# Optimization experiments

Measured on AMD Instinct MI355X. Metric: run time of the kernel, lower is better.

The kernel has to match this reference:

```python
import jax, jax.numpy as jnp
import numpy as np

BATCH, SEQ, HIDDEN = 8, 4096, 1024

def setup_inputs() -> dict:
    key = jax.random.key(0)
    hidden_states = jax.random.normal(key, (BATCH, SEQ, HIDDEN), dtype=jnp.float32)
    return {"hidden_states": hidden_states}

def reference(hidden_states) -> jnp.ndarray:
    # FFT along the sequence axis with orthonormal normalization (1/sqrt(N)),
    # then keep only the real part (FNet-style Fourier token mixing).
    fft_out = jnp.fft.fft(hidden_states, axis=1, norm="ortho")
    return jnp.real(fft_out).astype(hidden_states.dtype)
```

## Files before the change

### kernel.cpp

```cpp
#include <hip/hip_runtime.h>
#include <hip/hip_fp16.h>


static constexpr int SEQ = 4096;
static constexpr int HID = 1024;

struct alignas(8) h2x2 { __half2 a, b; };

__device__ __forceinline__ int rev4_3(int r) {
    return ((r & 3) << 4) | (r & 12) | ((r >> 4) & 3);
}


__device__ __forceinline__ void fft8(float* xr, float* xi) {
    const float C = 0.70710678118654752f;
    float ar[8], ai[8];
    ar[0] = xr[0] + xr[4];  ai[0] = xi[0] + xi[4];
    ar[1] = xr[0] - xr[4];  ai[1] = xi[0] - xi[4];
    ar[2] = xr[2] + xr[6];  ai[2] = xi[2] + xi[6];
    ar[3] = xr[2] - xr[6];  ai[3] = xi[2] - xi[6];
    ar[4] = xr[1] + xr[5];  ai[4] = xi[1] + xi[5];
    ar[5] = xr[1] - xr[5];  ai[5] = xi[1] - xi[5];
    ar[6] = xr[3] + xr[7];  ai[6] = xi[3] + xi[7];
    ar[7] = xr[3] - xr[7];  ai[7] = xi[3] - xi[7];
    float br[8], bi[8];
    br[0] = ar[0] + ar[2];  bi[0] = ai[0] + ai[2];
    br[2] = ar[0] - ar[2];  bi[2] = ai[0] - ai[2];
    br[1] = ar[1] + ai[3];  bi[1] = ai[1] - ar[3];
    br[3] = ar[1] - ai[3];  bi[3] = ai[1] + ar[3];
    br[4] = ar[4] + ar[6];  bi[4] = ai[4] + ai[6];
    br[6] = ar[4] - ar[6];  bi[6] = ai[4] - ai[6];
    br[5] = ar[5] + ai[7];  bi[5] = ai[5] - ar[7];
    br[7] = ar[5] - ai[7];  bi[7] = ai[5] + ar[7];
    const float t0r = br[4],                 t0i = bi[4];
    const float t1r = C * (br[5] + bi[5]),   t1i = C * (bi[5] - br[5]);
    const float t2r = bi[6],                 t2i = -br[6];
    const float t3r = C * (bi[7] - br[7]),   t3i = -C * (br[7] + bi[7]);
    xr[0] = br[0] + t0r;  xi[0] = bi[0] + t0i;
    xr[4] = br[0] - t0r;  xi[4] = bi[0] - t0i;
    xr[1] = br[1] + t1r;  xi[1] = bi[1] + t1i;
    xr[5] = br[1] - t1r;  xi[5] = bi[1] - t1i;
    xr[2] = br[2] + t2r;  xi[2] = bi[2] + t2i;
    xr[6] = br[2] - t2r;  xi[6] = bi[2] - t2i;
    xr[3] = br[3] + t3r;  xi[3] = bi[3] + t3i;
    xr[7] = br[3] - t3r;  xi[7] = bi[3] - t3i;
}

__device__ __forceinline__ void twiddle_chain(float* xr, float* xi,
                                              const float wc, const float ws) {
    float cr = wc, ci = ws;
    #pragma unroll
    for (int k = 1; k < 8; ++k) {
        const float tr = xr[k] * cr - xi[k] * ci;
        xi[k] = xr[k] * ci + xi[k] * cr;
        xr[k] = tr;
        if (k < 7) {
            const float nr = cr * wc - ci * ws;
            const float ni = cr * ws + ci * wc;
            cr = nr;  ci = ni;
        }
    }
}


__global__ __launch_bounds__(256) void fft_pass1_r8(const float* __restrict__ x,
                                                    __half2* __restrict__ u) {
    __shared__ float2 zs[2112];
    const int t  = threadIdx.x;
    const int pc = blockIdx.x & 15;
    const int n2 = (blockIdx.x >> 4) & 63;
    const int b  = blockIdx.x >> 10;
    const int c  = t & 31;
    const int q  = t >> 5;

    const float* xb = x + (size_t)b * SEQ * HID + (size_t)(pc * 64 + 2 * c);
    float xr[8], xi[8];
    #pragma unroll
    for (int a = 0; a < 8; ++a) {
        const float2 v = *(const float2*)(xb + (size_t)(n2 + 64 * (8 * a + q)) * HID);
        xr[a] = v.x;  xi[a] = v.y;
    }
    fft8(xr, xi);
    {
        float wsn, wcs;
        __sincosf(-0.09817477042468103f * (float)q, &wsn, &wcs);
        twiddle_chain(xr, xi, wcs, wsn);
    }
    #pragma unroll
    for (int k = 0; k < 8; ++k)
        zs[(k * 8 + q) * 33 + c] = make_float2(xr[k], xi[k]);
    __syncthreads();
    #pragma unroll
    for (int r = 0; r < 8; ++r) {
        const float2 v = zs[(q * 8 + r) * 33 + c];
        xr[r] = v.x;  xi[r] = v.y;
    }
    fft8(xr, xi);

    const float tw = -1.5339807878856412e-3f;
    float w0c, w0s, wsc, wss;
    __sincosf(tw * (float)(n2 * q), &w0s, &w0c);
    __sincosf(tw * (float)(n2 * 8), &wss, &wsc);
    const float sc = 0.015625f;
    w0c *= sc;  w0s *= sc;
    __half2* ub = u + (size_t)b * SEQ * 512 + (size_t)(64 * n2 + q) * 512 + pc * 32 + c;
    #pragma unroll
    for (int kh = 0; kh < 8; ++kh) {
        const float orr = xr[kh] * w0c - xi[kh] * w0s;
        const float oii = xr[kh] * w0s + xi[kh] * w0c;
        ub[(size_t)(8 * kh) * 512] = __floats2half2_rn(orr, oii);
        if (kh < 7) {
            const float nc = w0c * wsc - w0s * wss;
            const float ns = w0c * wss + w0s * wsc;
            w0c = nc;  w0s = ns;
        }
    }
}

__global__ __launch_bounds__(256) void fft_pass2_r8(const __half2* __restrict__ u,
                                                    float* __restrict__ out) {
    __shared__ float2 vs[2176];
    const int t   = threadIdx.x;
    const int b   = blockIdx.x >> 10;
    const int idx = blockIdx.x & 1023;
    const __half2* ub = u   + (size_t)b * SEQ * 512;
    float*         ob = out + (size_t)b * SEQ * HID;
    const float scale = 0.5f;
    float xr[8], xi[8];

    if (idx < 992) {
        const int k1 = 1 + (idx >> 5);
        const int pc = idx & 31;
        const int ab = t >> 7;
        const int q  = (t >> 4) & 7;
        const int c  = t & 15;
        const int k1sel = ab ? 64 - k1 : k1;
        const int p  = pc * 16 + c;
        const __half2* up = ub + (size_t)k1sel * 512 + p;
        #pragma unroll
        for (int a = 0; a < 8; ++a) {
            const float2 v = __half22float2(up[(size_t)(64 * (8 * a + q)) * 512]);
            xr[a] = v.x;  xi[a] = v.y;
        }
        fft8(xr, xi);
        {
            float wsn, wcs;
            __sincosf(-0.09817477042468103f * (float)q, &wsn, &wcs);
            twiddle_chain(xr, xi, wcs, wsn);
        }
        const int base = ab * 64;
        #pragma unroll
        for (int k = 0; k < 8; ++k)
            vs[(base + k * 8 + q) * 17 + c] = make_float2(xr[k], xi[k]);
        __syncthreads();
        #pragma unroll
        for (int r = 0; r < 8; ++r) {
            const float2 v = vs[(base + q * 8 + r) * 17 + c];
            xr[r] = v.x;  xi[r] = v.y;
        }
        fft8(xr, xi);
        __syncthreads();
        #pragma unroll
        for (int k = 0; k < 8; ++k)
            vs[(base + k * 8 + q) * 17 + c] = make_float2(xr[k], xi[k]);
        __syncthreads();
        float* op = ob + (size_t)k1sel * HID + 2 * p;
        #pragma unroll
        for (int kh = 0; kh < 8; ++kh) {
            const float2 pv = vs[((64 - base) + (7 - kh) * 8 + (7 - q)) * 17 + c];
            const int k2 = q + 8 * kh;
            *(float2*)(op + (size_t)(64 * k2) * HID) =
                make_float2((xr[kh] + pv.x) * scale, (xi[kh] + pv.y) * scale);
        }
    } else {
        const int s  = idx - 992;
        const int k1 = (s >> 4) * 32;
        const int pc = s & 15;
        const int q  = t >> 5;
        const int c  = t & 31;
        const int p  = pc * 32 + c;
        const __half2* up = ub + (size_t)k1 * 512 + p;
        #pragma unroll
        for (int a = 0; a < 8; ++a) {
            const float2 v = __half22float2(up[(size_t)(64 * (8 * a + q)) * 512]);
            xr[a] = v.x;  xi[a] = v.y;
        }
        fft8(xr, xi);
        {
            float wsn, wcs;
            __sincosf(-0.09817477042468103f * (float)q, &wsn, &wcs);
            twiddle_chain(xr, xi, wcs, wsn);
        }
        #pragma unroll
        for (int k = 0; k < 8; ++k)
            vs[(k * 8 + q) * 33 + c] = make_float2(xr[k], xi[k]);
        __syncthreads();
        #pragma unroll
        for (int r = 0; r < 8; ++r) {
            const float2 v = vs[(q * 8 + r) * 33 + c];
            xr[r] = v.x;  xi[r] = v.y;
        }
        fft8(xr, xi);
        __syncthreads();
        #pragma unroll
        for (int k = 0; k < 8; ++k)
            vs[(k * 8 + q) * 33 + c] = make_float2(xr[k], xi[k]);
        __syncthreads();
        const int q2 = (k1 == 0) ? ((8 - q) & 7) : (7 - q);
        float* op = ob + (size_t)k1 * HID + 2 * p;
        #pragma unroll
        for (int kh = 0; kh < 8; ++kh) {
            const int kh2 = (k1 == 0 && q == 0) ? ((8 - kh) & 7) : (7 - kh);
            const float2 pv = vs[(kh2 * 8 + q2) * 33 + c];
            const int k2 = q + 8 * kh;
            *(float2*)(op + (size_t)(64 * k2) * HID) =
                make_float2((xr[kh] + pv.x) * scale, (xi[kh] + pv.y) * scale);
        }
    }
}


template <int MC>
__device__ __forceinline__ void fft64_lds(float* re, float* im, int off, int stride, int mbase) {
    #pragma unroll
    for (int s = 0; s < 3; ++s) {
        const int L = 1 << (2 * s);
        const float ang = -6.283185307179586f / (float)(4 * L);
        #pragma unroll
        for (int mi = 0; mi < MC; ++mi) {
            const int m  = mbase + mi;
            const int j  = m & (L - 1);
            const int i0 = ((m >> (2 * s)) << (2 * s + 2)) + j;
            const int a0 = (i0        ) * stride + off;
            const int a1 = (i0 +     L) * stride + off;
            const int a2 = (i0 + 2 * L) * stride + off;
            const int a3 = (i0 + 3 * L) * stride + off;
            const float e0x = re[a0], e0y = im[a0];
            const float e1x = re[a1], e1y = im[a1];
            const float e2x = re[a2], e2y = im[a2];
            const float e3x = re[a3], e3y = im[a3];
            float w1s, w1c;
            __sincosf(ang * (float)j, &w1s, &w1c);
            const float w2c = w1c * w1c - w1s * w1s, w2s = 2.f * w1c * w1s;
            const float w3c = w2c * w1c - w2s * w1s, w3s = w2c * w1s + w2s * w1c;
            const float t1x = e1x * w1c - e1y * w1s, t1y = e1x * w1s + e1y * w1c;
            const float t2x = e2x * w2c - e2y * w2s, t2y = e2x * w2s + e2y * w2c;
            const float t3x = e3x * w3c - e3y * w3s, t3y = e3x * w3s + e3y * w3c;
            const float a02x = e0x + t2x, a02y = e0y + t2y;
            const float s02x = e0x - t2x, s02y = e0y - t2y;
            const float a13x = t1x + t3x, a13y = t1y + t3y;
            const float s13x = t1x - t3x, s13y = t1y - t3y;
            re[a0] = a02x + a13x;  im[a0] = a02y + a13y;
            re[a1] = s02x + s13y;  im[a1] = s02y - s13x;
            re[a2] = a02x - a13x;  im[a2] = a02y - a13y;
            re[a3] = s02x - s13y;  im[a3] = s02y + s13x;
        }
        __syncthreads();
    }
}

__global__ __launch_bounds__(256) void fft_pass1(const float* __restrict__ x,
                                                 float* __restrict__ out) {
    __shared__ float sre[64 * 65];
    __shared__ float sim[64 * 65];
    const int t  = threadIdx.x;
    const int pc = blockIdx.x & 7;
    const int n2 = (blockIdx.x >> 3) & 63;
    const int b  = blockIdx.x >> 9;
    const float* xb = x   + (size_t)b * SEQ * HID + pc * 128;
    float*       ob = out + (size_t)b * SEQ * HID + pc * 128;

    const int c  = t & 31;
    const int r0 = t >> 5;
    #pragma unroll
    for (int i = 0; i < 8; ++i) {
        const int r  = r0 + 8 * i;
        const float4 f = *(const float4*)(xb + (size_t)(n2 + 64 * r) * HID + 4 * c);
        const int rr = rev4_3(r);
        sre[rr * 65 + 2 * c]     = f.x;  sim[rr * 65 + 2 * c]     = f.y;
        sre[rr * 65 + 2 * c + 1] = f.z;  sim[rr * 65 + 2 * c + 1] = f.w;
    }
    __syncthreads();

    fft64_lds<4>(sre, sim, t & 63, 65, 4 * (t >> 6));

    const float tw = -1.5339807878856412e-3f;
    #pragma unroll
    for (int i = 0; i < 8; ++i) {
        const int k1 = r0 + 8 * i;
        float ws, wc;
        __sincosf(tw * (float)(n2 * k1), &ws, &wc);
        const float ar = sre[k1 * 65 + 2 * c],     ai = sim[k1 * 65 + 2 * c];
        const float br = sre[k1 * 65 + 2 * c + 1], bi = sim[k1 * 65 + 2 * c + 1];
        float4 f;
        f.x = ar * wc - ai * ws;  f.y = ar * ws + ai * wc;
        f.z = br * wc - bi * ws;  f.w = br * ws + bi * wc;
        *(float4*)(ob + (size_t)(64 * n2 + k1) * HID + 4 * c) = f;
    }
}

__global__ __launch_bounds__(256) void fft_pass2(float* out) {
    __shared__ float lds[8448];
    const int t   = threadIdx.x;
    const int b   = blockIdx.x >> 9;
    const int idx = blockIdx.x & 511;
    float* ob = out + (size_t)b * SEQ * HID;
    const float scale = 1.0f / 128.0f;

    if (idx < 496) {
        const int k1 = 1 + (idx >> 4);
        const int pc = idx & 15;
        float* are = lds;          float* aim = lds + 2112;
        float* bre = lds + 4224;   float* bim = lds + 6336;
        const int c  = t & 15;
        const int rg = t >> 4;
        #pragma unroll
        for (int i = 0; i < 4; ++i) {
            const int n2 = rg + 16 * i;
            const int rr = rev4_3(n2);
            const float4 fa = *(const float4*)(ob + (size_t)(64 * n2 + k1)      * HID + pc * 64 + 4 * c);
            const float4 fb = *(const float4*)(ob + (size_t)(64 * n2 + 64 - k1) * HID + pc * 64 + 4 * c);
            are[rr * 33 + 2 * c]     = fa.x;  aim[rr * 33 + 2 * c]     = fa.y;
            are[rr * 33 + 2 * c + 1] = fa.z;  aim[rr * 33 + 2 * c + 1] = fa.w;
            bre[rr * 33 + 2 * c]     = fb.x;  bim[rr * 33 + 2 * c]     = fb.y;
            bre[rr * 33 + 2 * c + 1] = fb.z;  bim[rr * 33 + 2 * c + 1] = fb.w;
        }
        __syncthreads();

        const int lane = t & 63;
        float* fre = lds + 4224 * (lane >> 5);
        fft64_lds<4>(fre, fre + 2112, lane & 31, 33, 4 * (t >> 6));

        #pragma unroll
        for (int i = 0; i < 4; ++i) {
            const int k2 = rg + 16 * i;
            const int q  = 63 - k2;
            float4 f, g;
            f.x = (are[k2 * 33 + 2 * c]     + bre[q * 33 + 2 * c])     * scale;
            f.y = (aim[k2 * 33 + 2 * c]     + bim[q * 33 + 2 * c])     * scale;
            f.z = (are[k2 * 33 + 2 * c + 1] + bre[q * 33 + 2 * c + 1]) * scale;
            f.w = (aim[k2 * 33 + 2 * c + 1] + bim[q * 33 + 2 * c + 1]) * scale;
            *(float4*)(ob + (size_t)(k1 + 64 * k2)      * HID + pc * 64 + 4 * c) = f;
            g.x = (bre[k2 * 33 + 2 * c]     + are[q * 33 + 2 * c])     * scale;
            g.y = (bim[k2 * 33 + 2 * c]     + aim[q * 33 + 2 * c])     * scale;
            g.z = (bre[k2 * 33 + 2 * c + 1] + are[q * 33 + 2 * c + 1]) * scale;
            g.w = (bim[k2 * 33 + 2 * c + 1] + aim[q * 33 + 2 * c + 1]) * scale;
            *(float4*)(ob + (size_t)(64 - k1 + 64 * k2) * HID + pc * 64 + 4 * c) = g;
        }
    } else {
        const int s  = idx - 496;
        const int k1 = (s >> 3) * 32;
        const int pc = s & 7;
        float* sre = lds;
        float* sim = lds + 4160;
        const int c  = t & 31;
        const int rg = t >> 5;
        #pragma unroll
        for (int i = 0; i < 8; ++i) {
            const int n2 = rg + 8 * i;
            const int rr = rev4_3(n2);
            const float4 f = *(const float4*)(ob + (size_t)(64 * n2 + k1) * HID + pc * 128 + 4 * c);
            sre[rr * 65 + 2 * c]     = f.x;  sim[rr * 65 + 2 * c]     = f.y;
            sre[rr * 65 + 2 * c + 1] = f.z;  sim[rr * 65 + 2 * c + 1] = f.w;
        }
        __syncthreads();

        fft64_lds<4>(sre, sim, t & 63, 65, 4 * (t >> 6));

        #pragma unroll
        for (int i = 0; i < 8; ++i) {
            const int k2 = rg + 8 * i;
            const int q  = (k1 == 0) ? ((64 - k2) & 63) : (63 - k2);
            float4 f;
            f.x = (sre[k2 * 65 + 2 * c]     + sre[q * 65 + 2 * c])     * scale;
            f.y = (sim[k2 * 65 + 2 * c]     + sim[q * 65 + 2 * c])     * scale;
            f.z = (sre[k2 * 65 + 2 * c + 1] + sre[q * 65 + 2 * c + 1]) * scale;
            f.w = (sim[k2 * 65 + 2 * c + 1] + sim[q * 65 + 2 * c + 1]) * scale;
            *(float4*)(ob + (size_t)(k1 + 64 * k2) * HID + pc * 128 + 4 * c) = f;
        }
    }
}

extern "C" void kernel_launch(void* const* d_in, const int* in_sizes, int n_in,
                              void* d_out, int out_size, void* d_ws, size_t ws_size,
                              hipStream_t stream) {
    const float* x = (const float*)d_in[0];
    float* out = (float*)d_out;
    const size_t need = (size_t)8 * SEQ * 512 * sizeof(__half2);
    if (ws_size >= need) {
        __half2* u = (__half2*)d_ws;
        fft_pass1_r8<<<dim3(8 * 64 * 16), dim3(256), 0, stream>>>(x, u);
        fft_pass2_r8<<<dim3(8 * 1024), dim3(256), 0, stream>>>(u, out);
    } else {
        fft_pass1<<<dim3(8 * 64 * 8), dim3(256), 0, stream>>>(x, out);
        fft_pass2<<<dim3(8 * 512), dim3(256), 0, stream>>>(out);
    }
}
```

Baseline: 263.9 us.

## Process two columns per thread with wider vector loads and nontemporal stores

Both FFT passes now have each thread handle two complex columns (two packed pairs). This allows 16-byte float4 global loads and stores, and 8-byte half2x2 workspace accesses. Blocks grow to 512 threads with a min-blocks launch bound, and the LDS tiles are widened to float4 with adjusted padding. Nontemporal hints are added on the input loads and output stores. The aim is fewer, wider memory transactions on a bandwidth-bound kernel, at the cost of higher register pressure per thread and larger LDS per block.

```diff
diff --git a/kernel.cpp b/kernel.cpp
--- a/kernel.cpp
+++ b/kernel.cpp
@@ -6,6 +6,8 @@
 static constexpr int HID = 1024;
 
 struct alignas(8) h2x2 { __half2 a, b; };
+
+typedef float nv4 __attribute__((ext_vector_type(4)));
 
 __device__ __forceinline__ int rev4_3(int r) {
     return ((r & 3) << 4) | (r & 12) | ((r >> 4) & 3);
@@ -63,39 +65,50 @@
 }
 
 
-__global__ __launch_bounds__(256) void fft_pass1_r8(const float* __restrict__ x,
-                                                    __half2* __restrict__ u) {
-    __shared__ float2 zs[2112];
+__global__ __launch_bounds__(512, 4) void fft_pass1_x2(const float* __restrict__ x,
+                                                       __half2* __restrict__ u) {
+    __shared__ float4 zs[64 * 65];
     const int t  = threadIdx.x;
-    const int pc = blockIdx.x & 15;
-    const int n2 = (blockIdx.x >> 4) & 63;
-    const int b  = blockIdx.x >> 10;
-    const int c  = t & 31;
-    const int q  = t >> 5;
-
-    const float* xb = x + (size_t)b * SEQ * HID + (size_t)(pc * 64 + 2 * c);
-    float xr[8], xi[8];
-    #pragma unroll
-    for (int a = 0; a < 8; ++a) {
-        const float2 v = *(const float2*)(xb + (size_t)(n2 + 64 * (8 * a + q)) * HID);
-        xr[a] = v.x;  xi[a] = v.y;
-    }
-    fft8(xr, xi);
-    {
-        float wsn, wcs;
-        __sincosf(-0.09817477042468103f * (float)q, &wsn, &wcs);
-        twiddle_chain(xr, xi, wcs, wsn);
-    }
+    const int pc = blockIdx.x & 3;
+    const int n2 = (blockIdx.x >> 2) & 63;
+    const int b  = blockIdx.x >> 8;
+    const int c  = t & 63;
+    const int q  = t >> 6;
+
+    const float* xb = x + (size_t)b * SEQ * HID + (size_t)(pc * 256 + 4 * c);
+    nv4 raw[8];
+    #pragma unroll
+    for (int a = 0; a < 8; ++a)
+        raw[a] = __builtin_nontemporal_load(
+            (const nv4*)(xb + (size_t)(n2 + 64 * (8 * a + q)) * HID));
+
+    float wq_s, wq_c;
+    __sincosf(-0.09817477042468103f * (float)q, &wq_s, &wq_c);
+
+    float fr0[8], fi0[8], fr1[8], fi1[8];
+    #pragma unroll
+    for (int a = 0; a < 8; ++a) { fr0[a] = raw[a].x; fi0[a] = raw[a].y; }
+    fft8(fr0, fi0);
+    twiddle_chain(fr0, fi0, wq_c, wq_s);
+    #pragma unroll
+    for (int a = 0; a < 8; ++a) { fr1[a] = raw[a].z; fi1[a] = raw[a].w; }
+    fft8(fr1, fi1);
+    twiddle_chain(fr1, fi1, wq_c, wq_s);
+
     #pragma unroll
     for (int k = 0; k < 8; ++k)
-        zs[(k * 8 + q) * 33 + c] = make_float2(xr[k], xi[k]);
+        zs[(k * 8 + q) * 65 + c] = make_float4(fr0[k], fi0[k], fr1[k], fi1[k]);
     __syncthreads();
-    #pragma unroll
-    for (int r = 0; r < 8; ++r) {
-        const float2 v = zs[(q * 8 + r) * 33 + c];
-        xr[r] = v.x;  xi[r] = v.y;
-    }
-    fft8(xr, xi);
+    float4 rw[8];
+    #pragma unroll
+    for (int r = 0; r < 8; ++r) rw[r] = zs[(q * 8 + r) * 65 + c];
+
+    #pragma unroll
+    for (int a = 0; a < 8; ++a) { fr0[a] = rw[a].x; fi0[a] = rw[a].y; }
+    fft8(fr0, fi0);
+    #pragma unroll
+    for (int a = 0; a < 8; ++a) { fr1[a] = rw[a].z; fi1[a] = rw[a].w; }
+    fft8(fr1, fi1);
 
     const float tw = -1.5339807878856412e-3f;
     float w0c, w0s, wsc, wss;
@@ -103,12 +116,15 @@
     __sincosf(tw * (float)(n2 * 8), &wss, &wsc);
     const float sc = 0.015625f;
     w0c *= sc;  w0s *= sc;
-    __half2* ub = u + (size_t)b * SEQ * 512 + (size_t)(64 * n2 + q) * 512 + pc * 32 + c;
+    __half2* ub = u + (size_t)b * SEQ * 512 + (size_t)(64 * n2 + q) * 512 + pc * 128 + 2 * c;
     #pragma unroll
     for (int kh = 0; kh < 8; ++kh) {
-        const float orr = xr[kh] * w0c - xi[kh] * w0s;
-        const float oii = xr[kh] * w0s + xi[kh] * w0c;
-        ub[(size_t)(8 * kh) * 512] = __floats2half2_rn(orr, oii);
+        h2x2 o;
+        o.a = __floats2half2_rn(fr0[kh] * w0c - fi0[kh] * w0s,
+                                fr0[kh] * w0s + fi0[kh] * w0c);
+        o.b = __floats2half2_rn(fr1[kh] * w0c - fi1[kh] * w0s,
+                                fr1[kh] * w0s + fi1[kh] * w0c);
+        *(h2x2*)(ub + (size_t)(8 * kh) * 512) = o;
         if (kh < 7) {
             const float nc = w0c * wsc - w0s * wss;
             const float ns = w0c * wss + w0s * wsc;
@@ -117,104 +133,142 @@
     }
 }
 
-__global__ __launch_bounds__(256) void fft_pass2_r8(const __half2* __restrict__ u,
-                                                    float* __restrict__ out) {
-    __shared__ float2 vs[2176];
+__global__ __launch_bounds__(512, 4) void fft_pass2_x2(const __half2* __restrict__ u,
+                                                       float* __restrict__ out) {
+    __shared__ float4 vs[128 * 33];
     const int t   = threadIdx.x;
-    const int b   = blockIdx.x >> 10;
-    const int idx = blockIdx.x & 1023;
+    const int b   = blockIdx.x >> 8;
+    const int idx = blockIdx.x & 255;
     const __half2* ub = u   + (size_t)b * SEQ * 512;
     float*         ob = out + (size_t)b * SEQ * HID;
     const float scale = 0.5f;
-    float xr[8], xi[8];
-
-    if (idx < 992) {
-        const int k1 = 1 + (idx >> 5);
-        const int pc = idx & 31;
-        const int ab = t >> 7;
-        const int q  = (t >> 4) & 7;
-        const int c  = t & 15;
+    float fr0[8], fi0[8], fr1[8], fi1[8];
+
+    if (idx < 248) {
+        const int k1 = 1 + (idx >> 3);
+        const int pc = idx & 7;
+        const int ab = t >> 8;
+        const int q  = (t >> 5) & 7;
+        const int c  = t & 31;
         const int k1sel = ab ? 64 - k1 : k1;
-        const int p  = pc * 16 + c;
+        const int p  = pc * 64 + 2 * c;
         const __half2* up = ub + (size_t)k1sel * 512 + p;
+        h2x2 raw[8];
+        #pragma unroll
+        for (int a = 0; a < 8; ++a)
+            raw[a] = *(const h2x2*)(up + (size_t)(64 * (8 * a + q)) * 512);
+
+        float wq_s, wq_c;
+        __sincosf(-0.09817477042468103f * (float)q, &wq_s, &wq_c);
         #pragma unroll
         for (int a = 0; a < 8; ++a) {
-            const float2 v = __half22float2(up[(size_t)(64 * (8 * a + q)) * 512]);
-            xr[a] = v.x;  xi[a] = v.y;
-        }
-        fft8(xr, xi);
-        {
-            float wsn, wcs;
-            __sincosf(-0.09817477042468103f * (float)q, &wsn, &wcs);
-            twiddle_chain(xr, xi, wcs, wsn);
-        }
+            const float2 v = __half22float2(raw[a].a);
+            fr0[a] = v.x;  fi0[a] = v.y;
+        }
+        fft8(fr0, fi0);
+        twiddle_chain(fr0, fi0, wq_c, wq_s);
+        #pragma unroll
+        for (int a = 0; a < 8; ++a) {
+            const float2 v = __half22float2(raw[a].b);
+            fr1[a] = v.x;  fi1[a] = v.y;
+        }
+        fft8(fr1, fi1);
+        twiddle_chain(fr1, fi1, wq_c, wq_s);
+
         const int base = ab * 64;
         #pragma unroll
         for (int k = 0; k < 8; ++k)
-            vs[(base + k * 8 + q) * 17 + c] = make_float2(xr[k], xi[k]);
-        __syncthreads();
-        #pragma unroll
-        for (int r = 0; r < 8; ++r) {
-            const float2 v = vs[(base + q * 8 + r) * 17 + c];
-            xr[r] = v.x;  xi[r] = v.y;
-        }
-        fft8(xr, xi);
+            vs[(base + k * 8 + q) * 33 + c] = make_float4(fr0[k], fi0[k], fr1[k], fi1[k]);
+        __syncthreads();
+        float4 rw[8];
+        #pragma unroll
+        for (int r = 0; r < 8; ++r) rw[r] = vs[(base + q * 8 + r) * 33 + c];
+        #pragma unroll
+        for (int a = 0; a < 8; ++a) { fr0[a] = rw[a].x; fi0[a] = rw[a].y; }
+        fft8(fr0, fi0);
+        #pragma unroll
+        for (int a = 0; a < 8; ++a) { fr1[a] = rw[a].z; fi1[a] = rw[a].w; }
+        fft8(fr1, fi1);
         __syncthreads();
         #pragma unroll
         for (int k = 0; k < 8; ++k)
-            vs[(base + k * 8 + q) * 17 + c] = make_float2(xr[k], xi[k]);
-        __syncthreads();
-        float* op = ob + (size_t)k1sel * HID + 2 * p;
+            vs[(base + k * 8 + q) * 33 + c] = make_float4(fr0[k], fi0[k], fr1[k], fi1[k]);
+        __syncthreads();
+
+        float* op = ob + (size_t)k1sel * HID + (size_t)(pc * 128 + 4 * c);
         #pragma unroll
         for (int kh = 0; kh < 8; ++kh) {
-            const float2 pv = vs[((64 - base) + (7 - kh) * 8 + (7 - q)) * 17 + c];
+            const float4 pv = vs[((64 - base) + (7 - kh) * 8 + (7 - q)) * 33 + c];
             const int k2 = q + 8 * kh;
-            *(float2*)(op + (size_t)(64 * k2) * HID) =
-                make_float2((xr[kh] + pv.x) * scale, (xi[kh] + pv.y) * scale);
+            nv4 o;
+            o.x = (fr0[kh] + pv.x) * scale;
+            o.y = (fi0[kh] + pv.y) * scale;
+            o.z = (fr1[kh] + pv.z) * scale;
+            o.w = (fi1[kh] + pv.w) * scale;
+            __builtin_nontemporal_store(o, (nv4*)(op + (size_t)(64 * k2) * HID));
         }
     } else {
-        const int s  = idx - 992;
-        const int k1 = (s >> 4) * 32;
-        const int pc = s & 15;
-        const int q  = t >> 5;
-        const int c  = t & 31;
-        const int p  = pc * 32 + c;
+        const int s  = idx - 248;
+        const int k1 = (s >> 2) * 32;
+        const int pc = s & 3;
+        const int q  = t >> 6;
+        const int c  = t & 63;
+        const int p  = pc * 128 + 2 * c;
         const __half2* up = ub + (size_t)k1 * 512 + p;
+        h2x2 raw[8];
+        #pragma unroll
+        for (int a = 0; a < 8; ++a)
+            raw[a] = *(const h2x2*)(up + (size_t)(64 * (8 * a + q)) * 512);
+
+        float wq_s, wq_c;
+        __sincosf(-0.09817477042468103f * (float)q, &wq_s, &wq_c);
         #pragma unroll
         for (int a = 0; a < 8; ++a) {
-            const float2 v = __half22float2(up[(size_t)(64 * (8 * a + q)) * 512]);
-            xr[a] = v.x;  xi[a] = v.y;
-        }
-        fft8(xr, xi);
-        {
-            float wsn, wcs;
-            __sincosf(-0.09817477042468103f * (float)q, &wsn, &wcs);
-            twiddle_chain(xr, xi, wcs, wsn);
-        }
+            const float2 v = __half22float2(raw[a].a);
+            fr0[a] = v.x;  fi0[a] = v.y;
+        }
+        fft8(fr0, fi0);
+        twiddle_chain(fr0, fi0, wq_c, wq_s);
+        #pragma unroll
+        for (int a = 0; a < 8; ++a) {
+            const float2 v = __half22float2(raw[a].b);
+            fr1[a] = v.x;  fi1[a] = v.y;
+        }
+        fft8(fr1, fi1);
+        twiddle_chain(fr1, fi1, wq_c, wq_s);
+
         #pragma unroll
         for (int k = 0; k < 8; ++k)
-            vs[(k * 8 + q) * 33 + c] = make_float2(xr[k], xi[k]);
-        __syncthreads();
-        #pragma unroll
-        for (int r = 0; r < 8; ++r) {
-            const float2 v = vs[(q * 8 + r) * 33 + c];
-            xr[r] = v.x;  xi[r] = v.y;
-        }
-        fft8(xr, xi);
+            vs[(k * 8 + q) * 65 + c] = make_float4(fr0[k], fi0[k], fr1[k], fi1[k]);
+        __syncthreads();
+        float4 rw[8];
+        #pragma unroll
+        for (int r = 0; r < 8; ++r) rw[r] = vs[(q * 8 + r) * 65 + c];
+        #pragma unroll
+        for (int a = 0; a < 8; ++a) { fr0[a] = rw[a].x; fi0[a] = rw[a].y; }
+        fft8(fr0, fi0);
+        #pragma unroll
+        for (int a = 0; a < 8; ++a) { fr1[a] = rw[a].z; fi1[a] = rw[a].w; }
+        fft8(fr1, fi1);
         __syncthreads();
         #pragma unroll
         for (int k = 0; k < 8; ++k)
-            vs[(k * 8 + q) * 33 + c] = make_float2(xr[k], xi[k]);
-        __syncthreads();
+            vs[(k * 8 + q) * 65 + c] = make_float4(fr0[k], fi0[k], fr1[k], fi1[k]);
+        __syncthreads();
+
         const int q2 = (k1 == 0) ? ((8 - q) & 7) : (7 - q);
-        float* op = ob + (size_t)k1 * HID + 2 * p;
+        float* op = ob + (size_t)k1 * HID + (size_t)(pc * 256 + 4 * c);
         #pragma unroll
         for (int kh = 0; kh < 8; ++kh) {
             const int kh2 = (k1 == 0 && q == 0) ? ((8 - kh) & 7) : (7 - kh);
-            const float2 pv = vs[(kh2 * 8 + q2) * 33 + c];
+            const float4 pv = vs[(kh2 * 8 + q2) * 65 + c];
             const int k2 = q + 8 * kh;
-            *(float2*)(op + (size_t)(64 * k2) * HID) =
-                make_float2((xr[kh] + pv.x) * scale, (xi[kh] + pv.y) * scale);
+            nv4 o;
+            o.x = (fr0[kh] + pv.x) * scale;
+            o.y = (fi0[kh] + pv.y) * scale;
+            o.z = (fr1[kh] + pv.z) * scale;
+            o.w = (fi1[kh] + pv.w) * scale;
+            __builtin_nontemporal_store(o, (nv4*)(op + (size_t)(64 * k2) * HID));
         }
     }
 }
@@ -389,8 +443,8 @@
     const size_t need = (size_t)8 * SEQ * 512 * sizeof(__half2);
     if (ws_size >= need) {
         __half2* u = (__half2*)d_ws;
-        fft_pass1_r8<<<dim3(8 * 64 * 16), dim3(256), 0, stream>>>(x, u);
-        fft_pass2_r8<<<dim3(8 * 1024), dim3(256), 0, stream>>>(u, out);
+        fft_pass1_x2<<<dim3(8 * 64 * 4), dim3(512), 0, stream>>>(x, u);
+        fft_pass2_x2<<<dim3(8 * 256), dim3(512), 0, stream>>>(u, out);
     } else {
         fft_pass1<<<dim3(8 * 64 * 8), dim3(256), 0, stream>>>(x, out);
         fft_pass2<<<dim3(8 * 512), dim3(256), 0, stream>>>(out);
```

New measurement: 240.2 us. 1.1x faster.
